# Optimization experiments

Hardware: AMD Instinct MI355X
Metric: run time of the kernel (lower is better)

Reference implementation:

```python
import jax, jax.numpy as jnp
import numpy as np

NEG_SLOPE = 0.2
BN_EPS = 1e-5


def _gat_conv(x, src, dst, W, a_src, a_dst, bias, heads, concat):
    # x: [N, Fin], W: [Fin, heads*C], a_src/a_dst: [heads, C]
    N = x.shape[0]
    C = W.shape[1] // heads
    h = (x @ W).reshape(N, heads, C)                       # [N, H, C]
    s_src = jnp.einsum('nhc,hc->nh', h, a_src)             # [N, H]
    s_dst = jnp.einsum('nhc,hc->nh', h, a_dst)             # [N, H]
    e = jax.nn.leaky_relu(s_src[src] + s_dst[dst], NEG_SLOPE)  # [E, H]
    # segment softmax over incoming edges of each destination node
    m = jax.ops.segment_max(e, dst, num_segments=N)
    m = jnp.where(jnp.isfinite(m), m, 0.0)
    ex = jnp.exp(e - m[dst])
    denom = jax.ops.segment_sum(ex, dst, num_segments=N)
    alpha = ex / (denom[dst] + 1e-16)                      # [E, H]
    out = jax.ops.segment_sum(alpha[:, :, None] * h[src], dst, num_segments=N)  # [N,H,C]
    if concat:
        out = out.reshape(N, heads * C)
    else:
        out = out.mean(axis=1)
    return out + bias


def setup_inputs() -> dict:
    key = jax.random.key(0)
    ks = jax.random.split(key, 12)
    N, E, Fin, Ch, H, Fout = 50000, 800000, 128, 32, 4, 2
    Fhid = Ch * H  # 128
    x = jax.random.normal(ks[0], (N, Fin), dtype=jnp.float32)
    edge_index = jax.random.randint(ks[1], (2, E), 0, N, dtype=jnp.int64)
    def glorot(k, shape):
        fan = shape[0] + shape[-1]
        return jax.random.normal(k, shape, dtype=jnp.float32) * jnp.sqrt(2.0 / fan)
    return {
        'x': x,
        'edge_index': edge_index,
        'W1': glorot(ks[2], (Fin, Fhid)),
        'att_src1': glorot(ks[3], (H, Ch)),
        'att_dst1': glorot(ks[4], (H, Ch)),
        'b1': jnp.zeros((Fhid,), jnp.float32),
        'gamma': jnp.ones((Fhid,), jnp.float32),
        'beta': jnp.zeros((Fhid,), jnp.float32),
        'W2': glorot(ks[5], (Fhid, Fout)),
        'att_src2': glorot(ks[6], (1, Fout)),
        'att_dst2': glorot(ks[7], (1, Fout)),
        'b2': jnp.zeros((Fout,), jnp.float32),
    }


def reference(x, edge_index, W1, att_src1, att_dst1, b1, gamma, beta,
              W2, att_src2, att_dst2, b2):
    N = x.shape[0]
    # PyG GATConv adds self-loops by default
    loops = jnp.arange(N, dtype=edge_index.dtype)
    src = jnp.concatenate([edge_index[0], loops])
    dst = jnp.concatenate([edge_index[1], loops])
    h = _gat_conv(x, src, dst, W1, att_src1, att_dst1, b1, heads=4, concat=True)
    # BatchNorm1d (batch statistics, train-mode math)
    mu = h.mean(axis=0)
    var = h.var(axis=0)
    h = (h - mu) * jax.lax.rsqrt(var + BN_EPS) * gamma + beta
    h = jax.nn.elu(h)
    # dropout = 0 (eval)
    out = _gat_conv(h, src, dst, W2, att_src2, att_dst2, b2, heads=1, concat=False)
    return out
```

## Files before the change

kernel.cpp:

```cpp
#include <hip/hip_runtime.h>
#include <hip/hip_bf16.h>
#include <hip/hip_fp16.h>
#include <math.h>

#define FH 128
#define NEG_SLOPE 0.2f
#define BN_EPS 1e-5f

__global__ __launch_bounds__(256) void k_gemm1(
    const float* __restrict__ x, const float* __restrict__ W,
    const float* __restrict__ asrc, const float* __restrict__ adst,
    __half* __restrict__ h1h, float* __restrict__ ssrc, float* __restrict__ sdst,
    int N)
{
    __shared__ float xs[64][132];
    __shared__ float Ws[128][64];
    const int t = threadIdx.x;
    const int row0 = blockIdx.x * 64;
    const int col0 = blockIdx.y * 64;

    #pragma unroll
    for (int i = 0; i < 8; ++i) {
        int f = (i * 256 + t) * 4;
        int r = f >> 7, c = f & 127;
        float4 v = make_float4(0.f, 0.f, 0.f, 0.f);
        if (row0 + r < N) v = *(const float4*)(x + (size_t)(row0 + r) * FH + c);
        xs[r][c] = v.x; xs[r][c + 1] = v.y; xs[r][c + 2] = v.z; xs[r][c + 3] = v.w;
    }
    #pragma unroll
    for (int i = 0; i < 8; ++i) {
        int f = (i * 256 + t) * 4;
        int k = f >> 6, c = f & 63;
        *(float4*)&Ws[k][c] = *(const float4*)(W + (size_t)k * FH + col0 + c);
    }
    __syncthreads();

    const int r  = t >> 3;
    const int cq = (t & 7) * 8;
    float accA[8] = {0,0,0,0,0,0,0,0};
    float accB[8] = {0,0,0,0,0,0,0,0};
    #pragma unroll 4
    for (int k = 0; k < 128; ++k) {
        float xa = xs[r][k];
        float xb = xs[r + 32][k];
        float4 w0 = *(const float4*)&Ws[k][cq];
        float4 w1 = *(const float4*)&Ws[k][cq + 4];
        accA[0] = fmaf(xa, w0.x, accA[0]); accA[1] = fmaf(xa, w0.y, accA[1]);
        accA[2] = fmaf(xa, w0.z, accA[2]); accA[3] = fmaf(xa, w0.w, accA[3]);
        accA[4] = fmaf(xa, w1.x, accA[4]); accA[5] = fmaf(xa, w1.y, accA[5]);
        accA[6] = fmaf(xa, w1.z, accA[6]); accA[7] = fmaf(xa, w1.w, accA[7]);
        accB[0] = fmaf(xb, w0.x, accB[0]); accB[1] = fmaf(xb, w0.y, accB[1]);
        accB[2] = fmaf(xb, w0.z, accB[2]); accB[3] = fmaf(xb, w0.w, accB[3]);
        accB[4] = fmaf(xb, w1.x, accB[4]); accB[5] = fmaf(xb, w1.y, accB[5]);
        accB[6] = fmaf(xb, w1.z, accB[6]); accB[7] = fmaf(xb, w1.w, accB[7]);
    }

    const int hg = (col0 >> 5) + (cq >> 5);
    const int cl = cq & 31;
    float4 as0 = *(const float4*)(asrc + hg * 32 + cl);
    float4 as1 = *(const float4*)(asrc + hg * 32 + cl + 4);
    float4 ad0 = *(const float4*)(adst + hg * 32 + cl);
    float4 ad1 = *(const float4*)(adst + hg * 32 + cl + 4);
    float sA = accA[0]*as0.x + accA[1]*as0.y + accA[2]*as0.z + accA[3]*as0.w
             + accA[4]*as1.x + accA[5]*as1.y + accA[6]*as1.z + accA[7]*as1.w;
    float dA = accA[0]*ad0.x + accA[1]*ad0.y + accA[2]*ad0.z + accA[3]*ad0.w
             + accA[4]*ad1.x + accA[5]*ad1.y + accA[6]*ad1.z + accA[7]*ad1.w;
    float sB = accB[0]*as0.x + accB[1]*as0.y + accB[2]*as0.z + accB[3]*as0.w
             + accB[4]*as1.x + accB[5]*as1.y + accB[6]*as1.z + accB[7]*as1.w;
    float dB = accB[0]*ad0.x + accB[1]*ad0.y + accB[2]*ad0.z + accB[3]*ad0.w
             + accB[4]*ad1.x + accB[5]*ad1.y + accB[6]*ad1.z + accB[7]*ad1.w;
    sA += __shfl_xor(sA, 1, 64); sA += __shfl_xor(sA, 2, 64);
    dA += __shfl_xor(dA, 1, 64); dA += __shfl_xor(dA, 2, 64);
    sB += __shfl_xor(sB, 1, 64); sB += __shfl_xor(sB, 2, 64);
    dB += __shfl_xor(dB, 1, 64); dB += __shfl_xor(dB, 2, 64);

    int ra = row0 + r, rb = row0 + r + 32;
    if (ra < N) {
        __half2 ph[4];
        ph[0] = __floats2half2_rn(accA[0], accA[1]);
        ph[1] = __floats2half2_rn(accA[2], accA[3]);
        ph[2] = __floats2half2_rn(accA[4], accA[5]);
        ph[3] = __floats2half2_rn(accA[6], accA[7]);
        *(uint4*)(h1h + (size_t)ra * FH + col0 + cq) = *(uint4*)ph;
        if ((t & 3) == 0) { ssrc[ra * 4 + hg] = sA; sdst[ra * 4 + hg] = dA; }
    }
    if (rb < N) {
        __half2 ph[4];
        ph[0] = __floats2half2_rn(accB[0], accB[1]);
        ph[1] = __floats2half2_rn(accB[2], accB[3]);
        ph[2] = __floats2half2_rn(accB[4], accB[5]);
        ph[3] = __floats2half2_rn(accB[6], accB[7]);
        *(uint4*)(h1h + (size_t)rb * FH + col0 + cq) = *(uint4*)ph;
        if ((t & 3) == 0) { ssrc[rb * 4 + hg] = sB; sdst[rb * 4 + hg] = dB; }
    }
}

__global__ void k_count(const int* __restrict__ ei, int E, int N, int* __restrict__ deg) {
    int i = blockIdx.x * blockDim.x + threadIdx.x;
    if (i >= E + N) return;
    int d = (i < E) ? ei[E + i] : (i - E);
    atomicAdd(&deg[d], 1);
}

__global__ __launch_bounds__(1024) void k_scan1(const int* __restrict__ deg,
                                                int* __restrict__ rowptr,
                                                int* __restrict__ blksum, int N) {
    int t = threadIdx.x;
    int i = blockIdx.x * 1024 + t;
    int v = (i < N) ? deg[i] : 0;
    int lane = t & 63, w = t >> 6;
    int incl = v;
    #pragma unroll
    for (int off = 1; off < 64; off <<= 1) {
        int tmp = __shfl_up(incl, off, 64);
        if (lane >= off) incl += tmp;
    }
    __shared__ int wsum[16];
    if (lane == 63) wsum[w] = incl;
    __syncthreads();
    if (t == 0) {
        int s = 0;
        for (int k = 0; k < 16; ++k) { int x = wsum[k]; wsum[k] = s; s += x; }
    }
    __syncthreads();
    int excl = incl - v + wsum[w];
    if (i < N) rowptr[i] = excl;
    if (t == 1023) blksum[blockIdx.x] = excl + v;
}

__global__ __launch_bounds__(1024) void k_scan2(const int* __restrict__ blksum,
                                                int* __restrict__ blkoff, int nblk) {
    int t = threadIdx.x;
    int v = (t < nblk) ? blksum[t] : 0;
    int lane = t & 63, w = t >> 6;
    int incl = v;
    #pragma unroll
    for (int off = 1; off < 64; off <<= 1) {
        int tmp = __shfl_up(incl, off, 64);
        if (lane >= off) incl += tmp;
    }
    __shared__ int wsum[16];
    if (lane == 63) wsum[w] = incl;
    __syncthreads();
    if (t == 0) {
        int s = 0;
        for (int k = 0; k < 16; ++k) { int x = wsum[k]; wsum[k] = s; s += x; }
    }
    __syncthreads();
    int excl = incl - v + wsum[w];
    if (t < nblk) blkoff[t] = excl;
    if (t == nblk - 1) blkoff[nblk] = excl + v;
}

__global__ void k_scan3(int* __restrict__ rowptr, const int* __restrict__ blkoff, int N) {
    int i = blockIdx.x * blockDim.x + threadIdx.x;
    if (i > N) return;
    if (i == N) rowptr[N] = blkoff[(N + 1023) >> 10];
    else        rowptr[i] += blkoff[i >> 10];
}

__global__ void k_fill(const int* __restrict__ ei, int E, int N,
                       const int* __restrict__ rowptr, int* __restrict__ deg,
                       int* __restrict__ csr) {
    int i = blockIdx.x * blockDim.x + threadIdx.x;
    if (i >= E + N) return;
    int s, d;
    if (i < E) { s = ei[i]; d = ei[E + i]; }
    else       { s = i - E; d = i - E; }
    int pos = atomicSub(&deg[d], 1) - 1;
    csr[rowptr[d] + pos] = s;
}

__global__ __launch_bounds__(256) void k_agg1(
    const int* __restrict__ rowptr, const int* __restrict__ csr,
    const __half* __restrict__ h1h, const float* __restrict__ ssrc,
    const float* __restrict__ sdst, const float* __restrict__ b1,
    float* __restrict__ out, int N)
{
    int n = (blockIdx.x * blockDim.x + threadIdx.x) >> 6;
    int lane = threadIdx.x & 63;
    if (n >= N) return;
    int start = rowptr[n];
    int dcnt  = rowptr[n + 1] - start;

    float4 sd4 = *(const float4*)(sdst + n * 4);
    float mx = -3e38f, my = -3e38f, mz = -3e38f, mw = -3e38f;
    for (int j = lane; j < dcnt; j += 64) {
        int s = csr[start + j];
        float4 sv = *(const float4*)(ssrc + s * 4);
        float ex = sv.x + sd4.x; ex = fmaxf(ex, NEG_SLOPE * ex);
        float ey = sv.y + sd4.y; ey = fmaxf(ey, NEG_SLOPE * ey);
        float ez = sv.z + sd4.z; ez = fmaxf(ez, NEG_SLOPE * ez);
        float ew = sv.w + sd4.w; ew = fmaxf(ew, NEG_SLOPE * ew);
        mx = fmaxf(mx, ex); my = fmaxf(my, ey);
        mz = fmaxf(mz, ez); mw = fmaxf(mw, ew);
    }
    #pragma unroll
    for (int off = 32; off; off >>= 1) {
        mx = fmaxf(mx, __shfl_xor(mx, off, 64));
        my = fmaxf(my, __shfl_xor(my, off, 64));
        mz = fmaxf(mz, __shfl_xor(mz, off, 64));
        mw = fmaxf(mw, __shfl_xor(mw, off, 64));
    }

    int h = lane >> 4;
    float Mh  = h == 0 ? mx : h == 1 ? my : h == 2 ? mz : mw;
    float sdh = h == 0 ? sd4.x : h == 1 ? sd4.y : h == 2 ? sd4.z : sd4.w;

    float ax = 0.f, ay = 0.f, l = 0.f;
    const __half2* h1v = (const __half2*)h1h;
    #pragma unroll 4
    for (int j = 0; j < dcnt; ++j) {
        int s = csr[start + j];
        float e = ssrc[s * 4 + h] + sdh;
        e = fmaxf(e, NEG_SLOPE * e);
        float p = __expf(e - Mh);
        l += p;
        float2 v = __half22float2(h1v[((size_t)s << 6) + lane]);
        ax = fmaf(p, v.x, ax);
        ay = fmaf(p, v.y, ay);
    }
    float inv = 1.f / (l + 1e-16f);
    float2 b1v = ((const float2*)b1)[lane];
    float2 o;
    o.x = fmaf(ax, inv, b1v.x);
    o.y = fmaf(ay, inv, b1v.y);
    ((float2*)out)[((size_t)n << 6) + lane] = o;
}

__global__ __launch_bounds__(256) void k_bnstat(const float4* __restrict__ hb4,
                                                float* __restrict__ bnsum,
                                                float* __restrict__ bnsq, int N) {
    __shared__ float rs[8][128];
    __shared__ float rq[8][128];
    int t = threadIdx.x;
    int rg = t >> 5, c4 = t & 31;
    float sx = 0, sy = 0, sz = 0, sw = 0, qx = 0, qy = 0, qz = 0, qw = 0;
    for (int r = blockIdx.x * 8 + rg; r < N; r += gridDim.x * 8) {
        float4 v = hb4[(size_t)r * 32 + c4];
        sx += v.x; sy += v.y; sz += v.z; sw += v.w;
        qx = fmaf(v.x, v.x, qx); qy = fmaf(v.y, v.y, qy);
        qz = fmaf(v.z, v.z, qz); qw = fmaf(v.w, v.w, qw);
    }
    int c = c4 * 4;
    rs[rg][c] = sx; rs[rg][c+1] = sy; rs[rg][c+2] = sz; rs[rg][c+3] = sw;
    rq[rg][c] = qx; rq[rg][c+1] = qy; rq[rg][c+2] = qz; rq[rg][c+3] = qw;
    __syncthreads();
    for (int k = 4; k; k >>= 1) {
        if (rg < k) {
            rs[rg][c]   += rs[rg+k][c];   rs[rg][c+1] += rs[rg+k][c+1];
            rs[rg][c+2] += rs[rg+k][c+2]; rs[rg][c+3] += rs[rg+k][c+3];
            rq[rg][c]   += rq[rg+k][c];   rq[rg][c+1] += rq[rg+k][c+1];
            rq[rg][c+2] += rq[rg+k][c+2]; rq[rg][c+3] += rq[rg+k][c+3];
        }
        __syncthreads();
    }
    if (t < 32) {
        int cc = t * 4;
        atomicAdd(&bnsum[cc],   rs[0][cc]);   atomicAdd(&bnsum[cc+1], rs[0][cc+1]);
        atomicAdd(&bnsum[cc+2], rs[0][cc+2]); atomicAdd(&bnsum[cc+3], rs[0][cc+3]);
        atomicAdd(&bnsq[cc],    rq[0][cc]);   atomicAdd(&bnsq[cc+1],  rq[0][cc+1]);
        atomicAdd(&bnsq[cc+2],  rq[0][cc+2]); atomicAdd(&bnsq[cc+3],  rq[0][cc+3]);
    }
}

__global__ __launch_bounds__(256) void k_bn2(const float4* __restrict__ hb4,
                                             const float* __restrict__ bnsum,
                                             const float* __restrict__ bnsq,
                                             const float* __restrict__ gamma,
                                             const float* __restrict__ beta,
                                             const float* __restrict__ W2,
                                             const float* __restrict__ as2,
                                             const float* __restrict__ ad2,
                                             float4* __restrict__ node2,
                                             int N, float invN) {
    int t = threadIdx.x;
    int rl = t >> 5, c4 = t & 31;
    int r = blockIdx.x * 8 + rl;
    if (r >= N) return;
    int c = c4 * 4;
    float4 s4 = *(const float4*)(bnsum + c);
    float4 q4 = *(const float4*)(bnsq + c);
    float4 g4 = *(const float4*)(gamma + c);
    float4 be4 = *(const float4*)(beta + c);
    float mu0 = s4.x * invN, mu1 = s4.y * invN, mu2 = s4.z * invN, mu3 = s4.w * invN;
    float sc0 = rsqrtf(q4.x * invN - mu0 * mu0 + BN_EPS) * g4.x;
    float sc1 = rsqrtf(q4.y * invN - mu1 * mu1 + BN_EPS) * g4.y;
    float sc2 = rsqrtf(q4.z * invN - mu2 * mu2 + BN_EPS) * g4.z;
    float sc3 = rsqrtf(q4.w * invN - mu3 * mu3 + BN_EPS) * g4.w;
    float sh0 = be4.x - mu0 * sc0, sh1 = be4.y - mu1 * sc1;
    float sh2 = be4.z - mu2 * sc2, sh3 = be4.w - mu3 * sc3;

    float4 v = hb4[(size_t)r * 32 + c4];
    float t0 = fmaf(v.x, sc0, sh0);
    float t1 = fmaf(v.y, sc1, sh1);
    float t2 = fmaf(v.z, sc2, sh2);
    float t3 = fmaf(v.w, sc3, sh3);
    t0 = t0 > 0.f ? t0 : expm1f(t0);
    t1 = t1 > 0.f ? t1 : expm1f(t1);
    t2 = t2 > 0.f ? t2 : expm1f(t2);
    t3 = t3 > 0.f ? t3 : expm1f(t3);
    float d0 = t0 * W2[c * 2]       + t1 * W2[(c + 1) * 2]
             + t2 * W2[(c + 2) * 2] + t3 * W2[(c + 3) * 2];
    float d1 = t0 * W2[c * 2 + 1]       + t1 * W2[(c + 1) * 2 + 1]
             + t2 * W2[(c + 2) * 2 + 1] + t3 * W2[(c + 3) * 2 + 1];
    #pragma unroll
    for (int off = 16; off; off >>= 1) {
        d0 += __shfl_xor(d0, off, 64);
        d1 += __shfl_xor(d1, off, 64);
    }
    if (c4 == 0) {
        float4 o;
        o.x = d0; o.y = d1;
        o.z = d0 * as2[0] + d1 * as2[1];
        o.w = d0 * ad2[0] + d1 * ad2[1];
        node2[r] = o;
    }
}

__global__ __launch_bounds__(256) void k_agg2(const int* __restrict__ rowptr,
                                              const int* __restrict__ csr,
                                              const float4* __restrict__ node2,
                                              const float* __restrict__ b2,
                                              float* __restrict__ out, int N) {
    int gid = blockIdx.x * blockDim.x + threadIdx.x;
    int n = gid >> 4;
    int ln = gid & 15;
    if (n >= N) return;
    int start = rowptr[n];
    int dcnt  = rowptr[n + 1] - start;
    float sdv = node2[n].w;
    float m = -3e38f, l = 0.f, a0 = 0.f, a1 = 0.f;
    for (int j = ln; j < dcnt; j += 16) {
        int s = csr[start + j];
        float4 hv = node2[s];
        float e = hv.z + sdv;
        e = fmaxf(e, NEG_SLOPE * e);
        float nm = fmaxf(m, e);
        float sc = __expf(m - nm);
        float p  = __expf(e - nm);
        a0 = a0 * sc + p * hv.x;
        a1 = a1 * sc + p * hv.y;
        l  = l * sc + p;
        m  = nm;
    }
    #pragma unroll
    for (int off = 8; off; off >>= 1) {
        float mo  = __shfl_xor(m, off, 64);
        float lo  = __shfl_xor(l, off, 64);
        float a0o = __shfl_xor(a0, off, 64);
        float a1o = __shfl_xor(a1, off, 64);
        float nm = fmaxf(m, mo);
        float sc = __expf(m - nm), so = __expf(mo - nm);
        l  = l * sc + lo * so;
        a0 = a0 * sc + a0o * so;
        a1 = a1 * sc + a1o * so;
        m  = nm;
    }
    if (ln == 0) {
        float inv = 1.f / (l + 1e-16f);
        float2 o;
        o.x = fmaf(a0, inv, b2[0]);
        o.y = fmaf(a1, inv, b2[1]);
        ((float2*)out)[n] = o;
    }
}

extern "C" void kernel_launch(void* const* d_in, const int* in_sizes, int n_in,
                              void* d_out, int out_size, void* d_ws, size_t ws_size,
                              hipStream_t stream) {
    const int N = in_sizes[0] / FH;
    const int E = in_sizes[1] / 2;
    const int Etot = E + N;
    const int nblk = (N + 1023) >> 10;

    const float* x     = (const float*)d_in[0];
    const int*   ei    = (const int*)d_in[1];
    const float* W1    = (const float*)d_in[2];
    const float* asrc1 = (const float*)d_in[3];
    const float* adst1 = (const float*)d_in[4];
    const float* b1    = (const float*)d_in[5];
    const float* gamma = (const float*)d_in[6];
    const float* beta  = (const float*)d_in[7];
    const float* W2    = (const float*)d_in[8];
    const float* as2   = (const float*)d_in[9];
    const float* ad2   = (const float*)d_in[10];
    const float* b2    = (const float*)d_in[11];
    float* out = (float*)d_out;

    char* ws = (char*)d_ws;
    size_t off = 0;
    auto nxt = [&](size_t bytes) {
        size_t o = off;
        off += (bytes + 255) & ~(size_t)255;
        return o;
    };
    __half* h1h    = (__half*)(ws + nxt((size_t)N * FH * 2));
    float* hb      = (float*)(ws + nxt((size_t)N * FH * 4));
    float* ssrc1   = (float*)(ws + nxt((size_t)N * 4 * 4));
    float* sdst1   = (float*)(ws + nxt((size_t)N * 4 * 4));
    float* node2   = (float*)(ws + nxt((size_t)N * 4 * 4));
    size_t zoff0   = off;
    int*   deg     = (int*)(ws + nxt((size_t)N * 4));
    float* bnsum   = (float*)(ws + nxt(128 * 4));
    float* bnsq    = (float*)(ws + nxt(128 * 4));
    size_t zbytes  = off - zoff0;
    int*   rowptr  = (int*)(ws + nxt((size_t)(N + 1) * 4));
    int*   csr     = (int*)(ws + nxt((size_t)Etot * 4));
    int*   blksum  = (int*)(ws + nxt((size_t)nblk * 4));
    int*   blkoff  = (int*)(ws + nxt((size_t)(nblk + 1) * 4));

    hipMemsetAsync(ws + zoff0, 0, zbytes, stream);

    dim3 g1((N + 63) / 64, 2);
    k_gemm1<<<g1, 256, 0, stream>>>(x, W1, asrc1, adst1, h1h, ssrc1, sdst1, N);
    k_count<<<(Etot + 255) / 256, 256, 0, stream>>>(ei, E, N, deg);
    k_scan1<<<nblk, 1024, 0, stream>>>(deg, rowptr, blksum, N);
    k_scan2<<<1, 1024, 0, stream>>>(blksum, blkoff, nblk);
    k_scan3<<<(N + 256) / 256, 256, 0, stream>>>(rowptr, blkoff, N);
    k_fill<<<(Etot + 255) / 256, 256, 0, stream>>>(ei, E, N, rowptr, deg, csr);
    k_agg1<<<(N + 3) / 4, 256, 0, stream>>>(rowptr, csr, h1h, ssrc1, sdst1, b1, hb, N);
    k_bnstat<<<512, 256, 0, stream>>>((const float4*)hb, bnsum, bnsq, N);
    k_bn2<<<(N + 7) / 8, 256, 0, stream>>>((const float4*)hb, bnsum, bnsq, gamma, beta,
                                           W2, as2, ad2, (float4*)node2, N,
                                           1.0f / (float)N);
    k_agg2<<<(N * 16 + 255) / 256, 256, 0, stream>>>(rowptr, csr, (const float4*)node2,
                                                     b2, out, N);
}
```

Baseline: 335.0 us.

## Precompute attention exponentials during CSR fill and retile layer-1 GEMM

The layer-1 GEMM is retiled to 256-row blocks with an 8x8 register tile per thread, k-chunked through a transposed shared-memory x tile, to raise arithmetic intensity. The CSR fill kernel now also computes leaky-relu attention logits and their exponentials per edge and stores them alongside the CSR indices. This removes the max pass and the per-edge score gathers from the layer-1 aggregation. The softmax max-subtraction is dropped, so exp overflow becomes possible for large logits, and there is an extra 16-byte-per-edge write and read.

```diff
diff --git a/kernel.cpp b/kernel.cpp
--- a/kernel.cpp
+++ b/kernel.cpp
@@ -13,85 +13,96 @@
     __half* __restrict__ h1h, float* __restrict__ ssrc, float* __restrict__ sdst,
     int N)
 {
-    __shared__ float xs[64][132];
-    __shared__ float Ws[128][64];
+    __shared__ float xsT[32][260];
+    __shared__ float Ws[32][68];
     const int t = threadIdx.x;
-    const int row0 = blockIdx.x * 64;
+    const int row0 = blockIdx.x * 256;
     const int col0 = blockIdx.y * 64;
-
-    #pragma unroll
-    for (int i = 0; i < 8; ++i) {
-        int f = (i * 256 + t) * 4;
-        int r = f >> 7, c = f & 127;
-        float4 v = make_float4(0.f, 0.f, 0.f, 0.f);
-        if (row0 + r < N) v = *(const float4*)(x + (size_t)(row0 + r) * FH + c);
-        xs[r][c] = v.x; xs[r][c + 1] = v.y; xs[r][c + 2] = v.z; xs[r][c + 3] = v.w;
-    }
-    #pragma unroll
-    for (int i = 0; i < 8; ++i) {
-        int f = (i * 256 + t) * 4;
-        int k = f >> 6, c = f & 63;
-        *(float4*)&Ws[k][c] = *(const float4*)(W + (size_t)k * FH + col0 + c);
-    }
-    __syncthreads();
-
-    const int r  = t >> 3;
-    const int cq = (t & 7) * 8;
-    float accA[8] = {0,0,0,0,0,0,0,0};
-    float accB[8] = {0,0,0,0,0,0,0,0};
-    #pragma unroll 4
-    for (int k = 0; k < 128; ++k) {
-        float xa = xs[r][k];
-        float xb = xs[r + 32][k];
-        float4 w0 = *(const float4*)&Ws[k][cq];
-        float4 w1 = *(const float4*)&Ws[k][cq + 4];
-        accA[0] = fmaf(xa, w0.x, accA[0]); accA[1] = fmaf(xa, w0.y, accA[1]);
-        accA[2] = fmaf(xa, w0.z, accA[2]); accA[3] = fmaf(xa, w0.w, accA[3]);
-        accA[4] = fmaf(xa, w1.x, accA[4]); accA[5] = fmaf(xa, w1.y, accA[5]);
-        accA[6] = fmaf(xa, w1.z, accA[6]); accA[7] = fmaf(xa, w1.w, accA[7]);
-        accB[0] = fmaf(xb, w0.x, accB[0]); accB[1] = fmaf(xb, w0.y, accB[1]);
-        accB[2] = fmaf(xb, w0.z, accB[2]); accB[3] = fmaf(xb, w0.w, accB[3]);
-        accB[4] = fmaf(xb, w1.x, accB[4]); accB[5] = fmaf(xb, w1.y, accB[5]);
-        accB[6] = fmaf(xb, w1.z, accB[6]); accB[7] = fmaf(xb, w1.w, accB[7]);
-    }
-
-    const int hg = (col0 >> 5) + (cq >> 5);
-    const int cl = cq & 31;
+    const int tc = t & 7, rg = t >> 3;
+    const int c0 = tc * 8, r0 = rg * 8;
+
+    float acc[8][8];
+    #pragma unroll
+    for (int i = 0; i < 8; ++i)
+        #pragma unroll
+        for (int j = 0; j < 8; ++j) acc[i][j] = 0.f;
+
+    for (int kc = 0; kc < 128; kc += 32) {
+        #pragma unroll
+        for (int i = 0; i < 8; ++i) {
+            int f4 = i * 256 + t;
+            int r = f4 >> 3, kq = (f4 & 7) * 4;
+            float4 v = make_float4(0.f, 0.f, 0.f, 0.f);
+            if (row0 + r < N) v = *(const float4*)(x + (size_t)(row0 + r) * FH + kc + kq);
+            xsT[kq][r] = v.x; xsT[kq + 1][r] = v.y;
+            xsT[kq + 2][r] = v.z; xsT[kq + 3][r] = v.w;
+        }
+        #pragma unroll
+        for (int i = 0; i < 2; ++i) {
+            int f4 = i * 256 + t;
+            int k = f4 >> 4, cq = (f4 & 15) * 4;
+            *(float4*)&Ws[k][cq] = *(const float4*)(W + (size_t)(kc + k) * FH + col0 + cq);
+        }
+        __syncthreads();
+        #pragma unroll 4
+        for (int k = 0; k < 32; ++k) {
+            float4 xa0 = *(const float4*)&xsT[k][r0];
+            float4 xa1 = *(const float4*)&xsT[k][r0 + 4];
+            float4 wv0 = *(const float4*)&Ws[k][c0];
+            float4 wv1 = *(const float4*)&Ws[k][c0 + 4];
+            float xr[8] = {xa0.x, xa0.y, xa0.z, xa0.w, xa1.x, xa1.y, xa1.z, xa1.w};
+            float wc[8] = {wv0.x, wv0.y, wv0.z, wv0.w, wv1.x, wv1.y, wv1.z, wv1.w};
+            #pragma unroll
+            for (int i = 0; i < 8; ++i)
+                #pragma unroll
+                for (int j = 0; j < 8; ++j)
+                    acc[i][j] = fmaf(xr[i], wc[j], acc[i][j]);
+        }
+        __syncthreads();
+    }
+
+    const int hg = (col0 + c0) >> 5;
+    const int cl = (col0 + c0) & 31;
     float4 as0 = *(const float4*)(asrc + hg * 32 + cl);
     float4 as1 = *(const float4*)(asrc + hg * 32 + cl + 4);
     float4 ad0 = *(const float4*)(adst + hg * 32 + cl);
     float4 ad1 = *(const float4*)(adst + hg * 32 + cl + 4);
-    float sA = accA[0]*as0.x + accA[1]*as0.y + accA[2]*as0.z + accA[3]*as0.w
-             + accA[4]*as1.x + accA[5]*as1.y + accA[6]*as1.z + accA[7]*as1.w;
-    float dA = accA[0]*ad0.x + accA[1]*ad0.y + accA[2]*ad0.z + accA[3]*ad0.w
-             + accA[4]*ad1.x + accA[5]*ad1.y + accA[6]*ad1.z + accA[7]*ad1.w;
-    float sB = accB[0]*as0.x + accB[1]*as0.y + accB[2]*as0.z + accB[3]*as0.w
-             + accB[4]*as1.x + accB[5]*as1.y + accB[6]*as1.z + accB[7]*as1.w;
-    float dB = accB[0]*ad0.x + accB[1]*ad0.y + accB[2]*ad0.z + accB[3]*ad0.w
-             + accB[4]*ad1.x + accB[5]*ad1.y + accB[6]*ad1.z + accB[7]*ad1.w;
-    sA += __shfl_xor(sA, 1, 64); sA += __shfl_xor(sA, 2, 64);
-    dA += __shfl_xor(dA, 1, 64); dA += __shfl_xor(dA, 2, 64);
-    sB += __shfl_xor(sB, 1, 64); sB += __shfl_xor(sB, 2, 64);
-    dB += __shfl_xor(dB, 1, 64); dB += __shfl_xor(dB, 2, 64);
-
-    int ra = row0 + r, rb = row0 + r + 32;
-    if (ra < N) {
-        __half2 ph[4];
-        ph[0] = __floats2half2_rn(accA[0], accA[1]);
-        ph[1] = __floats2half2_rn(accA[2], accA[3]);
-        ph[2] = __floats2half2_rn(accA[4], accA[5]);
-        ph[3] = __floats2half2_rn(accA[6], accA[7]);
-        *(uint4*)(h1h + (size_t)ra * FH + col0 + cq) = *(uint4*)ph;
-        if ((t & 3) == 0) { ssrc[ra * 4 + hg] = sA; sdst[ra * 4 + hg] = dA; }
-    }
-    if (rb < N) {
-        __half2 ph[4];
-        ph[0] = __floats2half2_rn(accB[0], accB[1]);
-        ph[1] = __floats2half2_rn(accB[2], accB[3]);
-        ph[2] = __floats2half2_rn(accB[4], accB[5]);
-        ph[3] = __floats2half2_rn(accB[6], accB[7]);
-        *(uint4*)(h1h + (size_t)rb * FH + col0 + cq) = *(uint4*)ph;
-        if ((t & 3) == 0) { ssrc[rb * 4 + hg] = sB; sdst[rb * 4 + hg] = dB; }
+    float as[8] = {as0.x, as0.y, as0.z, as0.w, as1.x, as1.y, as1.z, as1.w};
+    float ad[8] = {ad0.x, ad0.y, ad0.z, ad0.w, ad1.x, ad1.y, ad1.z, ad1.w};
+    float sA[8], dA[8];
+    #pragma unroll
+    for (int i = 0; i < 8; ++i) {
+        float s = 0.f, d = 0.f;
+        #pragma unroll
+        for (int j = 0; j < 8; ++j) {
+            s = fmaf(acc[i][j], as[j], s);
+            d = fmaf(acc[i][j], ad[j], d);
+        }
+        sA[i] = s; dA[i] = d;
+    }
+    #pragma unroll
+    for (int i = 0; i < 8; ++i) {
+        sA[i] += __shfl_xor(sA[i], 1, 64); sA[i] += __shfl_xor(sA[i], 2, 64);
+        dA[i] += __shfl_xor(dA[i], 1, 64); dA[i] += __shfl_xor(dA[i], 2, 64);
+    }
+    if ((tc & 3) == 0) {
+        #pragma unroll
+        for (int i = 0; i < 8; ++i) {
+            int row = row0 + r0 + i;
+            if (row < N) { ssrc[row * 4 + hg] = sA[i]; sdst[row * 4 + hg] = dA[i]; }
+        }
+    }
+    #pragma unroll
+    for (int i = 0; i < 8; ++i) {
+        int row = row0 + r0 + i;
+        if (row < N) {
+            __half2 ph[4];
+            ph[0] = __floats2half2_rn(acc[i][0], acc[i][1]);
+            ph[1] = __floats2half2_rn(acc[i][2], acc[i][3]);
+            ph[2] = __floats2half2_rn(acc[i][4], acc[i][5]);
+            ph[3] = __floats2half2_rn(acc[i][6], acc[i][7]);
+            *(uint4*)(h1h + (size_t)row * FH + col0 + c0) = *(uint4*)ph;
+        }
     }
 }
 
@@ -161,64 +172,50 @@
 
 __global__ void k_fill(const int* __restrict__ ei, int E, int N,
                        const int* __restrict__ rowptr, int* __restrict__ deg,
-                       int* __restrict__ csr) {
+                       const float4* __restrict__ ssrc4, const float4* __restrict__ sdst4,
+                       int* __restrict__ csr, float4* __restrict__ alpha4) {
     int i = blockIdx.x * blockDim.x + threadIdx.x;
     if (i >= E + N) return;
     int s, d;
     if (i < E) { s = ei[i]; d = ei[E + i]; }
     else       { s = i - E; d = i - E; }
     int pos = atomicSub(&deg[d], 1) - 1;
-    csr[rowptr[d] + pos] = s;
+    int slot = rowptr[d] + pos;
+    csr[slot] = s;
+    float4 sv = ssrc4[s];
+    float4 dv = sdst4[d];
+    float ex = sv.x + dv.x; ex = fmaxf(ex, NEG_SLOPE * ex);
+    float ey = sv.y + dv.y; ey = fmaxf(ey, NEG_SLOPE * ey);
+    float ez = sv.z + dv.z; ez = fmaxf(ez, NEG_SLOPE * ez);
+    float ew = sv.w + dv.w; ew = fmaxf(ew, NEG_SLOPE * ew);
+    float4 a;
+    a.x = __expf(ex); a.y = __expf(ey); a.z = __expf(ez); a.w = __expf(ew);
+    alpha4[slot] = a;
 }
 
 __global__ __launch_bounds__(256) void k_agg1(
     const int* __restrict__ rowptr, const int* __restrict__ csr,
-    const __half* __restrict__ h1h, const float* __restrict__ ssrc,
-    const float* __restrict__ sdst, const float* __restrict__ b1,
-    float* __restrict__ out, int N)
+    const float* __restrict__ alph, const __half* __restrict__ h1h,
+    const float* __restrict__ b1, float* __restrict__ out, int N)
 {
     int n = (blockIdx.x * blockDim.x + threadIdx.x) >> 6;
     int lane = threadIdx.x & 63;
     if (n >= N) return;
     int start = rowptr[n];
     int dcnt  = rowptr[n + 1] - start;
-
-    float4 sd4 = *(const float4*)(sdst + n * 4);
-    float mx = -3e38f, my = -3e38f, mz = -3e38f, mw = -3e38f;
-    for (int j = lane; j < dcnt; j += 64) {
-        int s = csr[start + j];
-        float4 sv = *(const float4*)(ssrc + s * 4);
-        float ex = sv.x + sd4.x; ex = fmaxf(ex, NEG_SLOPE * ex);
-        float ey = sv.y + sd4.y; ey = fmaxf(ey, NEG_SLOPE * ey);
-        float ez = sv.z + sd4.z; ez = fmaxf(ez, NEG_SLOPE * ez);
-        float ew = sv.w + sd4.w; ew = fmaxf(ew, NEG_SLOPE * ew);
-        mx = fmaxf(mx, ex); my = fmaxf(my, ey);
-        mz = fmaxf(mz, ez); mw = fmaxf(mw, ew);
-    }
-    #pragma unroll
-    for (int off = 32; off; off >>= 1) {
-        mx = fmaxf(mx, __shfl_xor(mx, off, 64));
-        my = fmaxf(my, __shfl_xor(my, off, 64));
-        mz = fmaxf(mz, __shfl_xor(mz, off, 64));
-        mw = fmaxf(mw, __shfl_xor(mw, off, 64));
-    }
-
     int h = lane >> 4;
-    float Mh  = h == 0 ? mx : h == 1 ? my : h == 2 ? mz : mw;
-    float sdh = h == 0 ? sd4.x : h == 1 ? sd4.y : h == 2 ? sd4.z : sd4.w;
 
     float ax = 0.f, ay = 0.f, l = 0.f;
     const __half2* h1v = (const __half2*)h1h;
     #pragma unroll 4
     for (int j = 0; j < dcnt; ++j) {
-        int s = csr[start + j];
-        float e = ssrc[s * 4 + h] + sdh;
-        e = fmaxf(e, NEG_SLOPE * e);
-        float p = __expf(e - Mh);
-        l += p;
+        int idx = start + j;
+        int s = csr[idx];
+        float a = alph[idx * 4 + h];
+        l += a;
         float2 v = __half22float2(h1v[((size_t)s << 6) + lane]);
-        ax = fmaf(p, v.x, ax);
-        ay = fmaf(p, v.y, ay);
+        ax = fmaf(a, v.x, ax);
+        ay = fmaf(a, v.y, ay);
     }
     float inv = 1.f / (l + 1e-16f);
     float2 b1v = ((const float2*)b1)[lane];
@@ -400,6 +397,7 @@
     float* ssrc1   = (float*)(ws + nxt((size_t)N * 4 * 4));
     float* sdst1   = (float*)(ws + nxt((size_t)N * 4 * 4));
     float* node2   = (float*)(ws + nxt((size_t)N * 4 * 4));
+    float* alpha   = (float*)(ws + nxt((size_t)Etot * 4 * 4));
     size_t zoff0   = off;
     int*   deg     = (int*)(ws + nxt((size_t)N * 4));
     float* bnsum   = (float*)(ws + nxt(128 * 4));
@@ -412,14 +410,17 @@
 
     hipMemsetAsync(ws + zoff0, 0, zbytes, stream);
 
-    dim3 g1((N + 63) / 64, 2);
+    dim3 g1((N + 255) / 256, 2);
     k_gemm1<<<g1, 256, 0, stream>>>(x, W1, asrc1, adst1, h1h, ssrc1, sdst1, N);
     k_count<<<(Etot + 255) / 256, 256, 0, stream>>>(ei, E, N, deg);
     k_scan1<<<nblk, 1024, 0, stream>>>(deg, rowptr, blksum, N);
     k_scan2<<<1, 1024, 0, stream>>>(blksum, blkoff, nblk);
     k_scan3<<<(N + 256) / 256, 256, 0, stream>>>(rowptr, blkoff, N);
-    k_fill<<<(Etot + 255) / 256, 256, 0, stream>>>(ei, E, N, rowptr, deg, csr);
-    k_agg1<<<(N + 3) / 4, 256, 0, stream>>>(rowptr, csr, h1h, ssrc1, sdst1, b1, hb, N);
+    k_fill<<<(Etot + 255) / 256, 256, 0, stream>>>(ei, E, N, rowptr, deg,
+                                                   (const float4*)ssrc1,
+                                                   (const float4*)sdst1,
+                                                   csr, (float4*)alpha);
+    k_agg1<<<(N + 3) / 4, 256, 0, stream>>>(rowptr, csr, alpha, h1h, b1, hb, N);
     k_bnstat<<<512, 256, 0, stream>>>((const float4*)hb, bnsum, bnsq, N);
     k_bn2<<<(N + 7) / 8, 256, 0, stream>>>((const float4*)hb, bnsum, bnsq, gamma, beta,
                                            W2, as2, ad2, (float4*)node2, N,
```

Result: faster. 321.2 us (-4.1%).
